# Kernel optimization log

Hardware: AMD Instinct MI355X
Metric: run time of the kernel (lower is better)

## Reference

```python
import jax, jax.numpy as jnp
import numpy as np

EPS = 1e-5

def _bn(x, g, b):
    m = x.mean(axis=0)
    v = x.var(axis=0)  # biased, matches torch BN training normalization
    return g * (x - m) * jax.lax.rsqrt(v + EPS) + b

def _mlp(x, W1, b1, g1, be1, W2, b2, g2, be2):
    h = jax.nn.relu(_bn(x @ W1 + b1, g1, be1))
    return jax.nn.relu(_bn(h @ W2 + b2, g2, be2))

def setup_inputs() -> dict:
    key = jax.random.key(0)
    ks = jax.random.split(key, 12)
    n, e, d, de = 100000, 1600000, 128, 16
    def lin(k, fan_in, fan_out):
        bound = 1.0 / np.sqrt(fan_in)
        k1, k2 = jax.random.split(k)
        W = jax.random.uniform(k1, (fan_in, fan_out), jnp.float32, -bound, bound)
        b = jax.random.uniform(k2, (fan_out,), jnp.float32, -bound, bound)
        return W, b
    msg_W1, msg_b1 = lin(ks[0], 2 * d + de, d)
    msg_W2, msg_b2 = lin(ks[1], d, d)
    upd_W1, upd_b1 = lin(ks[2], 3 * d, d)
    upd_W2, upd_b2 = lin(ks[3], d, d)
    return {
        "h": jax.random.normal(ks[4], (n, d), jnp.float32),
        "edge_index": jax.random.randint(ks[5], (2, e), 0, n, jnp.int64),
        "edge_attr": jax.random.normal(ks[6], (e, de), jnp.float32),
        "msg_W1": msg_W1, "msg_b1": msg_b1,
        "msg_g1": jnp.ones((d,)), "msg_be1": jnp.zeros((d,)),
        "msg_W2": msg_W2, "msg_b2": msg_b2,
        "msg_g2": jnp.ones((d,)), "msg_be2": jnp.zeros((d,)),
        "upd_W1": upd_W1, "upd_b1": upd_b1,
        "upd_g1": jnp.ones((d,)), "upd_be1": jnp.zeros((d,)),
        "upd_W2": upd_W2, "upd_b2": upd_b2,
        "upd_g2": jnp.ones((d,)), "upd_be2": jnp.zeros((d,)),
    }

def reference(h, edge_index, edge_attr,
              msg_W1, msg_b1, msg_g1, msg_be1, msg_W2, msg_b2, msg_g2, msg_be2,
              upd_W1, upd_b1, upd_g1, upd_be1, upd_W2, upd_b2, upd_g2, upd_be2):
    alpha = 0.5
    n = h.shape[0]
    src = edge_index[0]
    dst = edge_index[1]
    h_i = h[src]  # (e, d)
    h_j = h[dst]  # (e, d)
    msg_args = (msg_W1, msg_b1, msg_g1, msg_be1, msg_W2, msg_b2, msg_g2, msg_be2)
    m_st = _mlp(jnp.concatenate([h_i, h_j, edge_attr], axis=-1), *msg_args)
    m_ts = _mlp(jnp.concatenate([h_j, h_i, edge_attr], axis=-1), *msg_args)
    # NOTE: original code scatters both directions by source nodes (faithful)
    a_st = jax.ops.segment_sum(m_st, src, num_segments=n)
    a_ts = jax.ops.segment_sum(m_ts, src, num_segments=n)
    upd_in = jnp.concatenate([h, alpha * a_st, (1.0 - alpha) * a_ts], axis=-1)
    return _mlp(upd_in, upd_W1, upd_b1, upd_g1, upd_be1, upd_W2, upd_b2, upd_g2, upd_be2)
```

## Files before the change

kernel.cpp:

```cpp
#include <hip/hip_runtime.h>

#define EPS_BN 1e-5f

typedef __bf16 bf16x8 __attribute__((ext_vector_type(8)));
typedef _Float16 h4 __attribute__((ext_vector_type(4)));
typedef _Float16 h8 __attribute__((ext_vector_type(8)));
typedef float f32x4 __attribute__((ext_vector_type(4)));
typedef unsigned short us8 __attribute__((ext_vector_type(8)));
typedef unsigned short us4 __attribute__((ext_vector_type(4)));
typedef unsigned int u32x4 __attribute__((ext_vector_type(4)));

__device__ __forceinline__ unsigned short f2bf(float x) {
  unsigned u = __builtin_bit_cast(unsigned, x);
  unsigned r = (u + 0x7fffu + ((u >> 16) & 1u)) >> 16;
  return (unsigned short)r;
}
__device__ __forceinline__ unsigned pack2bf(float a, float b) {
  return (unsigned)f2bf(a) | ((unsigned)f2bf(b) << 16);
}
__device__ __forceinline__ unsigned short f2h(float x) {
  return __builtin_bit_cast(unsigned short, (_Float16)x);
}
__device__ __forceinline__ unsigned pack2h(float a, float b) {
  return (unsigned)f2h(a) | ((unsigned)f2h(b) << 16);
}
__device__ __forceinline__ float ubf(unsigned short u) {
  return __builtin_bit_cast(float, (unsigned)u << 16);
}
__device__ __forceinline__ h4 relu4(h4 x) {
  h4 z = {(_Float16)0.f, (_Float16)0.f, (_Float16)0.f, (_Float16)0.f};
  return __builtin_elementwise_max(x, z);
}

__device__ __forceinline__ int fragidx(int k, int c) {
  int nf = c >> 4, lr = c & 15, ks = k >> 5, lq = (k >> 3) & 3, j = k & 7;
  return ((((nf << 2) + ks) << 6) | (lq << 4) | lr) * 8 + j;
}

__global__ __launch_bounds__(256) void prep_all(
    const float* __restrict__ mW1, const float* __restrict__ mW2,
    const float* __restrict__ uW1, const float* __restrict__ uW2,
    unsigned short* __restrict__ wfrag) {
  int b = blockIdx.x;
  if (b == 7) {
    const float* s7 = mW1 + 256 * 128;
    unsigned short* oc = wfrag + 7L * 16384;
    for (int i = threadIdx.x; i < 2048; i += 256) oc[i] = f2h(s7[i]);
    return;
  }
  const float* src;
  float sc = 1.f;
  switch (b) {
    case 0: src = mW1; break;
    case 1: src = mW1 + 16384; break;
    case 2: src = mW2; break;
    case 3: src = uW1; break;
    case 4: src = uW1 + 16384; sc = 0.5f; break;
    case 5: src = uW1 + 32768; sc = 0.5f; break;
    default: src = uW2; break;
  }
  unsigned short* oc = wfrag + (long)b * 16384;
  bool fp16 = (b == 2);
  for (int i = threadIdx.x; i < 16384; i += 256) {
    float v = src[i] * sc;
    oc[fragidx(i >> 7, i & 127)] = fp16 ? f2h(v) : f2bf(v);
  }
}

__global__ __launch_bounds__(256) void hist_kernel(
    const int* __restrict__ SRC, long E, int* __restrict__ counts) {
  long i = (long)blockIdx.x * 256 + threadIdx.x;
  long str = (long)gridDim.x * 256;
  for (; i < E; i += str) atomicAdd(&counts[SRC[i]], 1);
}

__global__ __launch_bounds__(256) void scan1(
    const int* __restrict__ counts, int n, int* __restrict__ tmp,
    int* __restrict__ bsum) {
  __shared__ int sd[256];
  int b = blockIdx.x, tid = threadIdx.x;
  int base = b * 1024 + tid * 4;
  int c[4], t = 0;
  #pragma unroll
  for (int j = 0; j < 4; ++j) {
    int idx = base + j;
    c[j] = (idx < n) ? counts[idx] : 0;
    t += c[j];
  }
  sd[tid] = t;
  __syncthreads();
  for (int off = 1; off < 256; off <<= 1) {
    int v = (tid >= off) ? sd[tid - off] : 0;
    __syncthreads();
    sd[tid] += v;
    __syncthreads();
  }
  int run = sd[tid] - t;
  #pragma unroll
  for (int j = 0; j < 4; ++j) {
    int idx = base + j;
    if (idx < n) tmp[idx] = run;
    run += c[j];
  }
  if (tid == 255) bsum[b] = sd[255];
}

__global__ __launch_bounds__(256) void scan2(int* __restrict__ bsum, int nb) {
  __shared__ int sd[256];
  int tid = threadIdx.x;
  int v = (tid < nb) ? bsum[tid] : 0;
  sd[tid] = v;
  __syncthreads();
  for (int off = 1; off < 256; off <<= 1) {
    int x = (tid >= off) ? sd[tid - off] : 0;
    __syncthreads();
    sd[tid] += x;
    __syncthreads();
  }
  if (tid < nb) bsum[tid] = sd[tid] - v;
}

__global__ __launch_bounds__(256) void scan3(
    const int* __restrict__ tmp, const int* __restrict__ bsum, int n,
    int* __restrict__ cursor) {
  int i = blockIdx.x * 256 + threadIdx.x;
  if (i < n) cursor[i] = tmp[i] + bsum[i >> 10];
}

__global__ __launch_bounds__(256) void permute_edges(
    const int* __restrict__ SRC, const int* __restrict__ DST,
    const float* __restrict__ EA, long E, int* __restrict__ cursor,
    int* __restrict__ sS, int* __restrict__ sD,
    unsigned short* __restrict__ EAh) {
  long i = (long)blockIdx.x * 256 + threadIdx.x;
  long str = (long)gridDim.x * 256;
  for (; i < E; i += str) {
    int s = SRC[i];
    int pos = atomicAdd(&cursor[s], 1);
    sS[pos] = s;
    sD[pos] = DST[i];
    const float4* ep = (const float4*)(EA + i * 16);
    float4 a = ep[0], b = ep[1], c = ep[2], d = ep[3];
    u32x4 lo, hi;
    lo[0] = pack2h(a.x, a.y); lo[1] = pack2h(a.z, a.w);
    lo[2] = pack2h(b.x, b.y); lo[3] = pack2h(b.z, b.w);
    hi[0] = pack2h(c.x, c.y); hi[1] = pack2h(c.z, c.w);
    hi[2] = pack2h(d.x, d.y); hi[3] = pack2h(d.z, d.w);
    *(u32x4*)(EAh + (long)pos * 16) = lo;
    *(u32x4*)(EAh + (long)pos * 16 + 8) = hi;
  }
}

__global__ __launch_bounds__(256) void node_mfma_pq(
    const float* __restrict__ h, const unsigned short* __restrict__ WfA,
    unsigned short* __restrict__ pqb, int n) {
  __shared__ unsigned short WT[16384];
  int tid = threadIdx.x;
  int lid = tid & 63, w = tid >> 6, lr = lid & 15, lq = lid >> 4;
  long rbase = (long)blockIdx.x * 64 + 16 * w;
  long r = rbase + lr;
  bool rv = (r < n);
  long rl = rv ? r : 0;
  const us8* WF8 = (const us8*)WT;

  bf16x8 af[4];
  const float* Ar = h + rl * 128;
  #pragma unroll
  for (int ks = 0; ks < 4; ++ks) {
    int e0 = 32 * ks + 8 * lq;
    float4 x = *(const float4*)(Ar + e0);
    float4 y = *(const float4*)(Ar + e0 + 4);
    u32x4 t;
    t[0] = pack2bf(x.x, x.y); t[1] = pack2bf(x.z, x.w);
    t[2] = pack2bf(y.x, y.y); t[3] = pack2bf(y.z, y.w);
    if (!rv) { t[0] = 0; t[1] = 0; t[2] = 0; t[3] = 0; }
    af[ks] = __builtin_bit_cast(bf16x8, t);
  }

  f32x4 accP[8], accQ[8];
  #pragma unroll
  for (int nf = 0; nf < 8; ++nf) {
    accP[nf] = f32x4{0.f, 0.f, 0.f, 0.f};
    accQ[nf] = f32x4{0.f, 0.f, 0.f, 0.f};
  }

  for (int i = tid; i < 2048; i += 256) ((us8*)WT)[i] = ((const us8*)WfA)[i];
  __syncthreads();
  #pragma unroll
  for (int nf = 0; nf < 8; ++nf) {
    #pragma unroll
    for (int ks = 0; ks < 4; ++ks) {
      bf16x8 bf = __builtin_bit_cast(bf16x8, WF8[(nf * 4 + ks) * 64 + lid]);
      accP[nf] = __builtin_amdgcn_mfma_f32_16x16x32_bf16(af[ks], bf, accP[nf], 0, 0, 0);
    }
  }
  __syncthreads();
  for (int i = tid; i < 2048; i += 256) ((us8*)WT)[i] = ((const us8*)(WfA + 16384))[i];
  __syncthreads();
  #pragma unroll
  for (int nf = 0; nf < 8; ++nf) {
    #pragma unroll
    for (int ks = 0; ks < 4; ++ks) {
      bf16x8 bf = __builtin_bit_cast(bf16x8, WF8[(nf * 4 + ks) * 64 + lid]);
      accQ[nf] = __builtin_amdgcn_mfma_f32_16x16x32_bf16(af[ks], bf, accQ[nf], 0, 0, 0);
    }
  }

  #pragma unroll
  for (int nf = 0; nf < 8; ++nf) {
    #pragma unroll
    for (int i = 0; i < 4; ++i) {
      long nd = rbase + 4 * lq + i;
      if (nd < n) {
        int ch = 16 * nf + lr;
        pqb[nd * 256 + ch] = f2h(accP[nf][i]);
        pqb[nd * 256 + 128 + ch] = f2h(accQ[nf][i]);
      }
    }
  }
}

template <bool ABF16>
__global__ __launch_bounds__(256) void node_mfma(
    const void* A0, const void* A1, const void* A2,
    const unsigned short* __restrict__ Wf,
    float* __restrict__ C, int n, int dostats,
    float* __restrict__ sum_out, float* __restrict__ ssq_out, int nk) {
  __shared__ unsigned short WT[16384];
  int tid = threadIdx.x;
  int lid = tid & 63, w = tid >> 6, lr = lid & 15, lq = lid >> 4;
  long rbase = (long)blockIdx.x * 64 + 16 * w;

  const void* As[3] = {A0, A1, A2};
  f32x4 acc[8];
  #pragma unroll
  for (int nf = 0; nf < 8; ++nf) acc[nf] = f32x4{0.f, 0.f, 0.f, 0.f};

  long r = rbase + lr;
  bool rv = (r < n);
  long rl = rv ? r : 0;
  const us8* WF8 = (const us8*)WT;

  for (int c = 0; c < nk; ++c) {
    if (c) __syncthreads();
    const us8* src = (const us8*)(Wf + (long)c * 16384);
    for (int i = tid; i < 2048; i += 256) ((us8*)WT)[i] = src[i];
    __syncthreads();

    bf16x8 af[4];
    if (ABF16) {
      const us8* Ar = (const us8*)((const unsigned short*)As[c] + rl * 128);
      #pragma unroll
      for (int ks = 0; ks < 4; ++ks) {
        us8 v = Ar[ks * 4 + lq];
        if (!rv) v = us8{0, 0, 0, 0, 0, 0, 0, 0};
        af[ks] = __builtin_bit_cast(bf16x8, v);
      }
    } else {
      const float* Ar = (const float*)As[c] + rl * 128;
      #pragma unroll
      for (int ks = 0; ks < 4; ++ks) {
        int e0 = 32 * ks + 8 * lq;
        float4 x = *(const float4*)(Ar + e0);
        float4 y = *(const float4*)(Ar + e0 + 4);
        u32x4 t;
        t[0] = pack2bf(x.x, x.y); t[1] = pack2bf(x.z, x.w);
        t[2] = pack2bf(y.x, y.y); t[3] = pack2bf(y.z, y.w);
        if (!rv) { t[0] = 0; t[1] = 0; t[2] = 0; t[3] = 0; }
        af[ks] = __builtin_bit_cast(bf16x8, t);
      }
    }
    #pragma unroll
    for (int nf = 0; nf < 8; ++nf) {
      #pragma unroll
      for (int ks = 0; ks < 4; ++ks) {
        bf16x8 bf = __builtin_bit_cast(bf16x8, WF8[(nf * 4 + ks) * 64 + lid]);
        acc[nf] = __builtin_amdgcn_mfma_f32_16x16x32_bf16(af[ks], bf, acc[nf], 0, 0, 0);
      }
    }
  }

  float lsum[8], lssq[8];
  #pragma unroll
  for (int nf = 0; nf < 8; ++nf) { lsum[nf] = 0.f; lssq[nf] = 0.f; }
  #pragma unroll
  for (int nf = 0; nf < 8; ++nf) {
    #pragma unroll
    for (int i = 0; i < 4; ++i) {
      long nd = rbase + 4 * lq + i;
      if (nd < n) {
        float v = acc[nf][i];
        C[nd * 128 + 16 * nf + lr] = v;
        lsum[nf] += v; lssq[nf] += v * v;
      }
    }
  }
  if (dostats) {
    #pragma unroll
    for (int nf = 0; nf < 8; ++nf) {
      float v0 = lsum[nf]; v0 += __shfl_xor(v0, 16); v0 += __shfl_xor(v0, 32);
      float v1 = lssq[nf]; v1 += __shfl_xor(v1, 16); v1 += __shfl_xor(v1, 32);
      if (lq == 0) {
        atomicAdd(&sum_out[16 * nf + lr], v0);
        atomicAdd(&ssq_out[16 * nf + lr], v1);
      }
    }
  }
}

__global__ __launch_bounds__(256) void msg_stats1b(
    const unsigned short* __restrict__ PQ,
    const unsigned short* __restrict__ EAh, const float* __restrict__ W1e,
    const int* __restrict__ SRC, const int* __restrict__ DST, long E,
    float* __restrict__ stats) {
  __shared__ float Wel[16][128];
  __shared__ float red[32][16];
  int tid = threadIdx.x;
  for (int i = tid; i < 16 * 128; i += 256) ((float*)Wel)[i] = W1e[i];
  for (int i = tid; i < 512; i += 256) ((float*)red)[i] = 0.f;
  __syncthreads();
  int c4 = tid & 31, grp = tid >> 5;
  float4 s_st = {0,0,0,0}, q_st = {0,0,0,0}, s_ts = {0,0,0,0}, q_ts = {0,0,0,0};
  long stride = (long)gridDim.x * 8;
  for (long e = (long)blockIdx.x * 8 + grp; e < E; e += stride) {
    int s = SRC[e], t = DST[e];
    const unsigned short* Rs = PQ + (long)s * 256;
    const unsigned short* Rt = PQ + (long)t * 256;
    h4 Ps = __builtin_bit_cast(h4, *(const us4*)(Rs + 4 * c4));
    h4 Qs = __builtin_bit_cast(h4, *(const us4*)(Rs + 128 + 4 * c4));
    h4 Pt = __builtin_bit_cast(h4, *(const us4*)(Rt + 4 * c4));
    h4 Qt = __builtin_bit_cast(h4, *(const us4*)(Rt + 128 + 4 * c4));
    h8 elo = __builtin_bit_cast(h8, *(const us8*)(EAh + e * 16));
    h8 ehi = __builtin_bit_cast(h8, *(const us8*)(EAh + e * 16 + 8));
    float rx = 0.f, ry = 0.f, rz = 0.f, rw = 0.f;
    #pragma unroll
    for (int k = 0; k < 16; ++k) {
      float f = (k < 8) ? (float)elo[k & 7] : (float)ehi[k & 7];
      const float4 w4 = *(const float4*)&Wel[k][c4 * 4];
      rx = fmaf(f, w4.x, rx); ry = fmaf(f, w4.y, ry);
      rz = fmaf(f, w4.z, rz); rw = fmaf(f, w4.w, rw);
    }
    float zx = (float)Ps[0] + (float)Qt[0] + rx, zy = (float)Ps[1] + (float)Qt[1] + ry;
    float zz = (float)Ps[2] + (float)Qt[2] + rz, zw = (float)Ps[3] + (float)Qt[3] + rw;
    s_st.x += zx; s_st.y += zy; s_st.z += zz; s_st.w += zw;
    q_st.x += zx * zx; q_st.y += zy * zy; q_st.z += zz * zz; q_st.w += zw * zw;
    float ux = (float)Pt[0] + (float)Qs[0] + rx, uy = (float)Pt[1] + (float)Qs[1] + ry;
    float uz = (float)Pt[2] + (float)Qs[2] + rz, uw = (float)Pt[3] + (float)Qs[3] + rw;
    s_ts.x += ux; s_ts.y += uy; s_ts.z += uz; s_ts.w += uw;
    q_ts.x += ux * ux; q_ts.y += uy * uy; q_ts.z += uz * uz; q_ts.w += uw * uw;
  }
  atomicAdd(&red[c4][0], s_st.x);  atomicAdd(&red[c4][1], s_st.y);
  atomicAdd(&red[c4][2], s_st.z);  atomicAdd(&red[c4][3], s_st.w);
  atomicAdd(&red[c4][4], q_st.x);  atomicAdd(&red[c4][5], q_st.y);
  atomicAdd(&red[c4][6], q_st.z);  atomicAdd(&red[c4][7], q_st.w);
  atomicAdd(&red[c4][8], s_ts.x);  atomicAdd(&red[c4][9], s_ts.y);
  atomicAdd(&red[c4][10], s_ts.z); atomicAdd(&red[c4][11], s_ts.w);
  atomicAdd(&red[c4][12], q_ts.x); atomicAdd(&red[c4][13], q_ts.y);
  atomicAdd(&red[c4][14], q_ts.z); atomicAdd(&red[c4][15], q_ts.w);
  __syncthreads();
  #pragma unroll
  for (int rep = 0; rep < 2; ++rep) {
    int j = rep * 256 + tid;
    int cc = j >> 4, k = j & 15, group = k >> 2, comp = k & 3;
    atomicAdd(&stats[group * 128 + cc * 4 + comp], red[cc][k]);
  }
}

template <bool SCATTER>
__global__ __launch_bounds__(256) void msg_mfma10(
    const unsigned short* __restrict__ PQ,
    const unsigned short* __restrict__ EAh,
    const unsigned short* __restrict__ Weh,
    const unsigned short* __restrict__ W2f,
    const int* __restrict__ SRC, const int* __restrict__ DST, long E,
    const float* __restrict__ sc1, const float* __restrict__ sc2,
    float* __restrict__ stats2,
    float* __restrict__ a_st, float* __restrict__ a_ts) {
  __shared__ unsigned short W2F[16384];
  __shared__ unsigned short Atile[2][2][32][136];
  __shared__ int sArr[2][32];

  int tid = threadIdx.x;
  int c4 = tid & 31;
  int slot = tid >> 5;
  int lid = tid & 63, w = tid >> 6, lr = lid & 15, lq = lid >> 4;
  int dir = w >> 1;
  int half = (w & 1) * 16;

  for (int i = tid; i < 2048; i += 256) ((us8*)W2F)[i] = ((const us8*)W2f)[i];
  const us8* W2F8 = (const us8*)W2F;

  h4 wreg[16];
  #pragma unroll
  for (int k = 0; k < 16; ++k)
    wreg[k] = __builtin_bit_cast(h4, *(const us4*)(Weh + k * 128 + c4 * 4));

  int ch0 = c4 * 4;
  h4 scst4 = {(_Float16)sc1[ch0], (_Float16)sc1[ch0 + 1],
              (_Float16)sc1[ch0 + 2], (_Float16)sc1[ch0 + 3]};
  h4 shst4 = {(_Float16)sc1[128 + ch0], (_Float16)sc1[128 + ch0 + 1],
              (_Float16)sc1[128 + ch0 + 2], (_Float16)sc1[128 + ch0 + 3]};
  h4 scts4 = {(_Float16)sc1[256 + ch0], (_Float16)sc1[256 + ch0 + 1],
              (_Float16)sc1[256 + ch0 + 2], (_Float16)sc1[256 + ch0 + 3]};
  h4 shts4 = {(_Float16)sc1[384 + ch0], (_Float16)sc1[384 + ch0 + 1],
              (_Float16)sc1[384 + ch0 + 2], (_Float16)sc1[384 + ch0 + 3]};

  float s2[8], h2p[8];
  float ssum[8], sssq[8];
  if constexpr (SCATTER) {
    const float* scd = sc2 + dir * 256;
    #pragma unroll
    for (int nf = 0; nf < 8; ++nf) {
      int ch = 16 * nf + lr;
      s2[nf] = scd[ch]; h2p[nf] = scd[128 + ch];
    }
  } else {
    #pragma unroll
    for (int nf = 0; nf < 8; ++nf) { ssum[nf] = 0.f; sssq[nf] = 0.f; }
  }
  float* accOut = dir ? a_ts : a_st;

  long tb0 = (long)blockIdx.x * 32;
  long tstep = (long)gridDim.x * 32;

  auto phaseA = [&](long tb, int p) {
    int nE = (int)(E - tb < 32 ? E - tb : 32);
    #pragma unroll
    for (int rep = 0; rep < 4; ++rep) {
      int er = rep * 8 + slot;
      if (er < nE) {
        long e = tb + er;
        int s = SRC[e], t = DST[e];
        if (SCATTER && c4 == 0) sArr[p][er] = s;
        const us4* Rs = (const us4*)(PQ + (long)s * 256);
        const us4* Rt = (const us4*)(PQ + (long)t * 256);
        h4 Ps = __builtin_bit_cast(h4, Rs[c4]);
        h4 Qs = __builtin_bit_cast(h4, Rs[32 + c4]);
        h4 Pt = __builtin_bit_cast(h4, Rt[c4]);
        h4 Qt = __builtin_bit_cast(h4, Rt[32 + c4]);
        h8 elo = __builtin_bit_cast(h8, *(const us8*)(EAh + e * 16));
        h8 ehi = __builtin_bit_cast(h8, *(const us8*)(EAh + e * 16 + 8));
        h4 r = {(_Float16)0.f, (_Float16)0.f, (_Float16)0.f, (_Float16)0.f};
        #pragma unroll
        for (int k = 0; k < 16; ++k) {
          _Float16 f = (k < 8) ? elo[k & 7] : ehi[k & 7];
          h4 fv = {f, f, f, f};
          r += fv * wreg[k];
        }
        h4 zst = relu4((Ps + Qt + r) * scst4 + shst4);
        h4 zts = relu4((Pt + Qs + r) * scts4 + shts4);
        *(unsigned long long*)&Atile[p][0][er][ch0] =
            __builtin_bit_cast(unsigned long long, zst);
        *(unsigned long long*)&Atile[p][1][er][ch0] =
            __builtin_bit_cast(unsigned long long, zts);
      } else {
        *(unsigned long long*)&Atile[p][0][er][ch0] = 0ull;
        *(unsigned long long*)&Atile[p][1][er][ch0] = 0ull;
      }
    }
  };

  if (tb0 < E) phaseA(tb0, 0);
  __syncthreads();

  int p = 0;
  for (long tb = tb0; tb < E; tb += tstep) {
    int nE = (int)(E - tb < 32 ? E - tb : 32);
    long tnext = tb + tstep;

    int arow = half + lr;
    const char* ap = (const char*)&Atile[p][dir][arow][0];
    int acolb = lq * 16;
    h8 af[4];
    #pragma unroll
    for (int ks = 0; ks < 4; ++ks) {
      af[ks] = *(const h8*)(ap + ks * 64 + acolb);
    }
    int srow[4];
    bool uniform = false;
    int usrc = -1;
    if constexpr (SCATTER) {
      #pragma unroll
      for (int i = 0; i < 4; ++i) {
        int row = half + 4 * lq + i;
        srow[i] = (row < nE) ? sArr[p][row] : -1;
      }
      if (half + 15 < nE) {
        usrc = sArr[p][half];
        uniform = (usrc == sArr[p][half + 15]);
      }
    }
    f32x4 acc[8];
    __builtin_amdgcn_s_setprio(1);
    #pragma unroll
    for (int nf = 0; nf < 8; ++nf) {
      acc[nf] = f32x4{0.f, 0.f, 0.f, 0.f};
      #pragma unroll
      for (int ks = 0; ks < 4; ++ks) {
        h8 bf = __builtin_bit_cast(h8, W2F8[(nf * 4 + ks) * 64 + lid]);
        acc[nf] = __builtin_amdgcn_mfma_f32_16x16x32_f16(af[ks], bf, acc[nf], 0, 0, 0);
      }
    }
    __builtin_amdgcn_s_setprio(0);

    if (tnext < E) phaseA(tnext, p ^ 1);

    #pragma unroll
    for (int nf = 0; nf < 8; ++nf) {
      if constexpr (SCATTER) {
        int ch = 16 * nf + lr;
        if (uniform) {
          float m = 0.f;
          #pragma unroll
          for (int i = 0; i < 4; ++i)
            m += fmaxf(fmaf(acc[nf][i], s2[nf], h2p[nf]), 0.f);
          m += __shfl_xor(m, 16);
          m += __shfl_xor(m, 32);
          if (lq == 0 && m != 0.f)
            atomicAdd(&accOut[(long)usrc * 128 + ch], m);
        } else {
          int cur = srow[0];
          float m = fmaxf(fmaf(acc[nf][0], s2[nf], h2p[nf]), 0.f);
          #pragma unroll
          for (int i = 1; i < 4; ++i) {
            float v = fmaxf(fmaf(acc[nf][i], s2[nf], h2p[nf]), 0.f);
            if (srow[i] == cur) {
              m += v;
            } else {
              if (cur >= 0 && m != 0.f) atomicAdd(&accOut[(long)cur * 128 + ch], m);
              cur = srow[i]; m = v;
            }
          }
          if (cur >= 0 && m != 0.f) atomicAdd(&accOut[(long)cur * 128 + ch], m);
        }
      } else {
        #pragma unroll
        for (int i = 0; i < 4; ++i) {
          ssum[nf] += acc[nf][i]; sssq[nf] += acc[nf][i] * acc[nf][i];
        }
      }
    }
    __syncthreads();
    p ^= 1;
  }

  if constexpr (!SCATTER) {
    #pragma unroll
    for (int nf = 0; nf < 8; ++nf) {
      float v0 = ssum[nf]; v0 += __shfl_xor(v0, 16); v0 += __shfl_xor(v0, 32);
      float v1 = sssq[nf]; v1 += __shfl_xor(v1, 16); v1 += __shfl_xor(v1, 32);
      if (lq == 0) {
        int ch = 16 * nf + lr;
        atomicAdd(&stats2[dir * 256 + ch], v0);
        atomicAdd(&stats2[dir * 256 + 128 + ch], v1);
      }
    }
  }
}

__global__ void bn_finalize(const float* __restrict__ sum, const float* __restrict__ ssq,
                            float invN, const float* __restrict__ g,
                            const float* __restrict__ be,
                            float* __restrict__ sc, float* __restrict__ sh) {
  int j = threadIdx.x;
  float m = sum[j] * invN;
  float v = ssq[j] * invN - m * m;
  float s = g[j] * rsqrtf(v + EPS_BN);
  sc[j] = s;
  sh[j] = be[j] - m * s;
}

__global__ __launch_bounds__(256) void prescale_relu(
    const float* __restrict__ X, const float* __restrict__ scsh,
    unsigned* __restrict__ out, long nrows) {
  long gid = (long)blockIdx.x * 256 + threadIdx.x;
  int c2 = (int)(gid & 63);
  float s0 = scsh[2 * c2], s1 = scsh[2 * c2 + 1];
  float h0 = scsh[128 + 2 * c2], h1 = scsh[128 + 2 * c2 + 1];
  const float2* X2 = (const float2*)X;
  long rstride = ((long)gridDim.x * 256) >> 6;
  for (long row = gid >> 6; row < nrows; row += rstride) {
    float2 x = X2[row * 64 + c2];
    out[row * 64 + c2] = pack2bf(fmaxf(fmaf(x.x, s0, h0), 0.f),
                                 fmaxf(fmaf(x.y, s1, h1), 0.f));
  }
}

__global__ __launch_bounds__(256) void bn_relu_out(
    const float* __restrict__ U2, const float* __restrict__ scsh,
    float* __restrict__ out, long total) {
  long i = (long)blockIdx.x * blockDim.x + threadIdx.x;
  long stride = (long)gridDim.x * blockDim.x;
  for (; i < total; i += stride) {
    int j = (int)(i & 127);
    out[i] = fmaxf(fmaf(U2[i], scsh[j], scsh[128 + j]), 0.f);
  }
}

extern "C" void kernel_launch(void* const* d_in, const int* in_sizes, int n_in,
                              void* d_out, int out_size, void* d_ws, size_t ws_size,
                              hipStream_t stream) {
  const float* h    = (const float*)d_in[0];
  const int*   ei   = (const int*)d_in[1];
  const float* ea   = (const float*)d_in[2];
  const float* mW1  = (const float*)d_in[3];
  const float* mg1  = (const float*)d_in[5];
  const float* mbe1 = (const float*)d_in[6];
  const float* mW2  = (const float*)d_in[7];
  const float* mg2  = (const float*)d_in[9];
  const float* mbe2 = (const float*)d_in[10];
  const float* uW1  = (const float*)d_in[11];
  const float* ug1  = (const float*)d_in[13];
  const float* ube1 = (const float*)d_in[14];
  const float* uW2  = (const float*)d_in[15];
  const float* ug2  = (const float*)d_in[17];
  const float* ube2 = (const float*)d_in[18];

  int n = in_sizes[0] / 128;
  long E = (long)(in_sizes[1] / 2);
  const int* SRC = ei;
  const int* DST = ei + E;
  const float* W1e = mW1 + 256 * 128;

  size_t nf = (size_t)n * 128;
  unsigned short* pqb = (unsigned short*)d_ws;
  float* a_st = (float*)(pqb + (size_t)n * 256);
  float* a_ts = a_st + nf;
  float* st   = a_ts + nf;
  unsigned short* wfrag = (unsigned short*)(st + 3072);
  unsigned short* wfA  = wfrag;
  unsigned short* wfW2 = wfrag + 2 * 16384;
  unsigned short* wfU1 = wfrag + 3 * 16384;
  unsigned short* wfU2 = wfrag + 6 * 16384;
  unsigned short* wfWe = wfrag + 7 * 16384;
  int* sS = (int*)(wfWe + 2048);
  int* sD = sS + E;
  unsigned short* EAh = (unsigned short*)(sD + E);
  int* counts = (int*)(EAh + (size_t)E * 16);
  int* tmp = counts + n;
  int* bsum = tmp + n;

  float invE = 1.0f / (float)E;
  float invN = 1.0f / (float)n;
  int nblk = (n + 63) / 64;
  int nb1 = (n + 1023) / 1024;

  prep_all<<<8, 256, 0, stream>>>(mW1, mW2, uW1, uW2, wfrag);
  hipMemsetAsync(st, 0, 3072 * sizeof(float), stream);
  hipMemsetAsync(a_st, 0, 2 * nf * sizeof(float), stream);
  hipMemsetAsync(counts, 0, (size_t)n * sizeof(int), stream);

  hist_kernel<<<1024, 256, 0, stream>>>(SRC, E, counts);
  scan1<<<nb1, 256, 0, stream>>>(counts, n, tmp, bsum);
  scan2<<<1, 256, 0, stream>>>(bsum, nb1);
  scan3<<<(n + 255) / 256, 256, 0, stream>>>(tmp, bsum, n, counts);
  permute_edges<<<1024, 256, 0, stream>>>(SRC, DST, ea, E, counts, sS, sD, EAh);

  node_mfma_pq<<<nblk, 256, 0, stream>>>(h, wfA, pqb, n);

  msg_stats1b<<<2048, 256, 0, stream>>>(pqb, EAh, W1e, sS, sD, E, st);
  bn_finalize<<<1, 128, 0, stream>>>(st + 0,   st + 128, invE, mg1, mbe1, st + 1536, st + 1664);
  bn_finalize<<<1, 128, 0, stream>>>(st + 256, st + 384, invE, mg1, mbe1, st + 1792, st + 1920);

  msg_mfma10<false><<<1536, 256, 0, stream>>>(
      pqb, EAh, wfWe, wfW2, sS, sD, E, st + 1536, nullptr, st + 512, nullptr, nullptr);
  bn_finalize<<<1, 128, 0, stream>>>(st + 512, st + 640, invE, mg2, mbe2, st + 2048, st + 2176);
  bn_finalize<<<1, 128, 0, stream>>>(st + 768, st + 896, invE, mg2, mbe2, st + 2304, st + 2432);

  msg_mfma10<true><<<1536, 256, 0, stream>>>(
      pqb, EAh, wfWe, wfW2, sS, sD, E, st + 1536, st + 2048, nullptr, a_st, a_ts);

  float* u1 = (float*)pqb;
  node_mfma<false><<<nblk, 256, 0, stream>>>(h, a_st, a_ts, wfU1,
                                             u1, n, 1, st + 1024, st + 1152, 3);
  bn_finalize<<<1, 128, 0, stream>>>(st + 1024, st + 1152, invN, ug1, ube1, st + 2560, st + 2688);

  unsigned short* u1p = (unsigned short*)a_st;
  float* u2 = a_ts;
  prescale_relu<<<2048, 256, 0, stream>>>(u1, st + 2560, (unsigned*)u1p, n);
  node_mfma<true><<<nblk, 256, 0, stream>>>(u1p, nullptr, nullptr, wfU2,
                                            u2, n, 1, st + 1280, st + 1408, 1);
  bn_finalize<<<1, 128, 0, stream>>>(st + 1280, st + 1408, invN, ug2, ube2, st + 2816, st + 2944);

  bn_relu_out<<<2048, 256, 0, stream>>>(u2, st + 2816, (float*)d_out, (long)n * 128);
}
```

Measured before the change: 2.435 ms.

## Materialize second-layer message activations to avoid recomputing edge MLP for scatter

```diff
diff --git a/kernel.cpp b/kernel.cpp
--- a/kernel.cpp
+++ b/kernel.cpp
@@ -364,6 +364,184 @@
     int cc = j >> 4, k = j & 15, group = k >> 2, comp = k & 3;
     atomicAdd(&stats[group * 128 + cc * 4 + comp], red[cc][k]);
   }
+}
+
+__global__ __launch_bounds__(256) void msg_mfma11(
+    const unsigned short* __restrict__ PQ,
+    const unsigned short* __restrict__ EAh,
+    const unsigned short* __restrict__ Weh,
+    const unsigned short* __restrict__ W2f,
+    const int* __restrict__ SRC, const int* __restrict__ DST, long E,
+    const float* __restrict__ sc1, float* __restrict__ stats2,
+    unsigned short* __restrict__ ybuf) {
+  __shared__ unsigned short W2F[16384];
+  __shared__ unsigned short Atile[2][2][32][136];
+
+  int tid = threadIdx.x;
+  int c4 = tid & 31;
+  int slot = tid >> 5;
+  int lid = tid & 63, w = tid >> 6, lr = lid & 15, lq = lid >> 4;
+  int dir = w >> 1;
+  int half = (w & 1) * 16;
+
+  for (int i = tid; i < 2048; i += 256) ((us8*)W2F)[i] = ((const us8*)W2f)[i];
+  const us8* W2F8 = (const us8*)W2F;
+
+  h4 wreg[16];
+  #pragma unroll
+  for (int k = 0; k < 16; ++k)
+    wreg[k] = __builtin_bit_cast(h4, *(const us4*)(Weh + k * 128 + c4 * 4));
+
+  int ch0 = c4 * 4;
+  h4 scst4 = {(_Float16)sc1[ch0], (_Float16)sc1[ch0 + 1],
+              (_Float16)sc1[ch0 + 2], (_Float16)sc1[ch0 + 3]};
+  h4 shst4 = {(_Float16)sc1[128 + ch0], (_Float16)sc1[128 + ch0 + 1],
+              (_Float16)sc1[128 + ch0 + 2], (_Float16)sc1[128 + ch0 + 3]};
+  h4 scts4 = {(_Float16)sc1[256 + ch0], (_Float16)sc1[256 + ch0 + 1],
+              (_Float16)sc1[256 + ch0 + 2], (_Float16)sc1[256 + ch0 + 3]};
+  h4 shts4 = {(_Float16)sc1[384 + ch0], (_Float16)sc1[384 + ch0 + 1],
+              (_Float16)sc1[384 + ch0 + 2], (_Float16)sc1[384 + ch0 + 3]};
+
+  float ssum[8], sssq[8];
+  #pragma unroll
+  for (int nf = 0; nf < 8; ++nf) { ssum[nf] = 0.f; sssq[nf] = 0.f; }
+
+  long tb0 = (long)blockIdx.x * 32;
+  long tstep = (long)gridDim.x * 32;
+
+  auto phaseA = [&](long tb, int p) {
+    int nE = (int)(E - tb < 32 ? E - tb : 32);
+    #pragma unroll
+    for (int rep = 0; rep < 4; ++rep) {
+      int er = rep * 8 + slot;
+      if (er < nE) {
+        long e = tb + er;
+        int s = SRC[e], t = DST[e];
+        const us4* Rs = (const us4*)(PQ + (long)s * 256);
+        const us4* Rt = (const us4*)(PQ + (long)t * 256);
+        h4 Ps = __builtin_bit_cast(h4, Rs[c4]);
+        h4 Qs = __builtin_bit_cast(h4, Rs[32 + c4]);
+        h4 Pt = __builtin_bit_cast(h4, Rt[c4]);
+        h4 Qt = __builtin_bit_cast(h4, Rt[32 + c4]);
+        h8 elo = __builtin_bit_cast(h8, *(const us8*)(EAh + e * 16));
+        h8 ehi = __builtin_bit_cast(h8, *(const us8*)(EAh + e * 16 + 8));
+        h4 r = {(_Float16)0.f, (_Float16)0.f, (_Float16)0.f, (_Float16)0.f};
+        #pragma unroll
+        for (int k = 0; k < 16; ++k) {
+          _Float16 f = (k < 8) ? elo[k & 7] : ehi[k & 7];
+          h4 fv = {f, f, f, f};
+          r += fv * wreg[k];
+        }
+        h4 zst = relu4((Ps + Qt + r) * scst4 + shst4);
+        h4 zts = relu4((Pt + Qs + r) * scts4 + shts4);
+        *(unsigned long long*)&Atile[p][0][er][ch0] =
+            __builtin_bit_cast(unsigned long long, zst);
+        *(unsigned long long*)&Atile[p][1][er][ch0] =
+            __builtin_bit_cast(unsigned long long, zts);
+      } else {
+        *(unsigned long long*)&Atile[p][0][er][ch0] = 0ull;
+        *(unsigned long long*)&Atile[p][1][er][ch0] = 0ull;
+      }
+    }
+  };
+
+  if (tb0 < E) phaseA(tb0, 0);
+  __syncthreads();
+
+  int p = 0;
+  for (long tb = tb0; tb < E; tb += tstep) {
+    int nE = (int)(E - tb < 32 ? E - tb : 32);
+    long tnext = tb + tstep;
+
+    int arow = half + lr;
+    const char* ap = (const char*)&Atile[p][dir][arow][0];
+    int acolb = lq * 16;
+    h8 af[4];
+    #pragma unroll
+    for (int ks = 0; ks < 4; ++ks) {
+      af[ks] = *(const h8*)(ap + ks * 64 + acolb);
+    }
+    f32x4 acc[8];
+    __builtin_amdgcn_s_setprio(1);
+    #pragma unroll
+    for (int nf = 0; nf < 8; ++nf) {
+      acc[nf] = f32x4{0.f, 0.f, 0.f, 0.f};
+      #pragma unroll
+      for (int ks = 0; ks < 4; ++ks) {
+        h8 bf = __builtin_bit_cast(h8, W2F8[(nf * 4 + ks) * 64 + lid]);
+        acc[nf] = __builtin_amdgcn_mfma_f32_16x16x32_f16(af[ks], bf, acc[nf], 0, 0, 0);
+      }
+    }
+    __builtin_amdgcn_s_setprio(0);
+
+    if (tnext < E) phaseA(tnext, p ^ 1);
+
+    #pragma unroll
+    for (int nf = 0; nf < 8; ++nf) {
+      int ch = 16 * nf + lr;
+      #pragma unroll
+      for (int i = 0; i < 4; ++i) {
+        float v = acc[nf][i];
+        ssum[nf] += v; sssq[nf] += v * v;
+        int row = half + 4 * lq + i;
+        if (row < nE) ybuf[(tb + row) * 256 + dir * 128 + ch] = f2h(v);
+      }
+    }
+    __syncthreads();
+    p ^= 1;
+  }
+
+  #pragma unroll
+  for (int nf = 0; nf < 8; ++nf) {
+    float v0 = ssum[nf]; v0 += __shfl_xor(v0, 16); v0 += __shfl_xor(v0, 32);
+    float v1 = sssq[nf]; v1 += __shfl_xor(v1, 16); v1 += __shfl_xor(v1, 32);
+    if (lq == 0) {
+      int ch = 16 * nf + lr;
+      atomicAdd(&stats2[dir * 256 + ch], v0);
+      atomicAdd(&stats2[dir * 256 + 128 + ch], v1);
+    }
+  }
+}
+
+__global__ __launch_bounds__(256) void scatter_stream(
+    const unsigned short* __restrict__ Y, const int* __restrict__ sS, long E,
+    const float* __restrict__ sc2,
+    float* __restrict__ a_st, float* __restrict__ a_ts) {
+  __shared__ unsigned short Yl[8][256];
+  __shared__ int Sl[8];
+  int tid = threadIdx.x;
+  int dir = tid >> 7, ch = tid & 127;
+  float s2 = sc2[dir * 256 + ch];
+  float h2 = sc2[dir * 256 + 128 + ch];
+  float* accOut = dir ? a_ts : a_st;
+  long eper = (E + gridDim.x - 1) / gridDim.x;
+  long e0 = (long)blockIdx.x * eper;
+  long e1 = e0 + eper; if (e1 > E) e1 = E;
+  int run_src = -1;
+  float run_acc = 0.f;
+  for (long cb = e0; cb < e1; cb += 8) {
+    int cnt = (int)((e1 - cb < 8) ? (e1 - cb) : 8);
+    int le = tid >> 5, lo = (tid & 31) * 8;
+    if (le < cnt)
+      *(us8*)&Yl[le][lo] = *(const us8*)(Y + (cb + le) * 256 + lo);
+    if (tid < cnt) Sl[tid] = sS[cb + tid];
+    __syncthreads();
+    for (int i = 0; i < cnt; ++i) {
+      float y = (float)__builtin_bit_cast(_Float16, Yl[i][dir * 128 + ch]);
+      float v = fmaxf(fmaf(y, s2, h2), 0.f);
+      int s = Sl[i];
+      if (s == run_src) {
+        run_acc += v;
+      } else {
+        if (run_src >= 0 && run_acc != 0.f)
+          atomicAdd(&accOut[(long)run_src * 128 + ch], run_acc);
+        run_src = s; run_acc = v;
+      }
+    }
+    __syncthreads();
+  }
+  if (run_src >= 0 && run_acc != 0.f)
+    atomicAdd(&accOut[(long)run_src * 128 + ch], run_acc);
 }
 
 template <bool SCATTER>
@@ -639,6 +817,9 @@
   int* counts = (int*)(EAh + (size_t)E * 16);
   int* tmp = counts + n;
   int* bsum = tmp + n;
+  unsigned short* ybuf = (unsigned short*)(bsum + 256);
+  size_t needY = (size_t)((char*)(ybuf + (size_t)E * 256) - (char*)d_ws);
+  bool matY = (ws_size >= needY);
 
   float invE = 1.0f / (float)E;
   float invN = 1.0f / (float)n;
@@ -662,13 +843,20 @@
   bn_finalize<<<1, 128, 0, stream>>>(st + 0,   st + 128, invE, mg1, mbe1, st + 1536, st + 1664);
   bn_finalize<<<1, 128, 0, stream>>>(st + 256, st + 384, invE, mg1, mbe1, st + 1792, st + 1920);
 
-  msg_mfma10<false><<<1536, 256, 0, stream>>>(
-      pqb, EAh, wfWe, wfW2, sS, sD, E, st + 1536, nullptr, st + 512, nullptr, nullptr);
-  bn_finalize<<<1, 128, 0, stream>>>(st + 512, st + 640, invE, mg2, mbe2, st + 2048, st + 2176);
-  bn_finalize<<<1, 128, 0, stream>>>(st + 768, st + 896, invE, mg2, mbe2, st + 2304, st + 2432);
-
-  msg_mfma10<true><<<1536, 256, 0, stream>>>(
-      pqb, EAh, wfWe, wfW2, sS, sD, E, st + 1536, st + 2048, nullptr, a_st, a_ts);
+  if (matY) {
+    msg_mfma11<<<1536, 256, 0, stream>>>(
+        pqb, EAh, wfWe, wfW2, sS, sD, E, st + 1536, st + 512, ybuf);
+    bn_finalize<<<1, 128, 0, stream>>>(st + 512, st + 640, invE, mg2, mbe2, st + 2048, st + 2176);
+    bn_finalize<<<1, 128, 0, stream>>>(st + 768, st + 896, invE, mg2, mbe2, st + 2304, st + 2432);
+    scatter_stream<<<2048, 256, 0, stream>>>(ybuf, sS, E, st + 2048, a_st, a_ts);
+  } else {
+    msg_mfma10<false><<<1536, 256, 0, stream>>>(
+        pqb, EAh, wfWe, wfW2, sS, sD, E, st + 1536, nullptr, st + 512, nullptr, nullptr);
+    bn_finalize<<<1, 128, 0, stream>>>(st + 512, st + 640, invE, mg2, mbe2, st + 2048, st + 2176);
+    bn_finalize<<<1, 128, 0, stream>>>(st + 768, st + 896, invE, mg2, mbe2, st + 2304, st + 2432);
+    msg_mfma10<true><<<1536, 256, 0, stream>>>(
+        pqb, EAh, wfWe, wfW2, sS, sD, E, st + 1536, st + 2048, nullptr, a_st, a_ts);
+  }
 
   float* u1 = (float*)pqb;
   node_mfma<false><<<nblk, 256, 0, stream>>>(h, a_st, a_ts, wfU1,
```

After: 2.426 ms. No clear change (-0.4%).

## Precompute edge-attribute projection into workspace buffer and use streamlined message kernels

Applied to the files above, without the earlier changes.

```diff
diff --git a/kernel.cpp b/kernel.cpp
--- a/kernel.cpp
+++ b/kernel.cpp
@@ -24,11 +24,13 @@
 __device__ __forceinline__ unsigned pack2h(float a, float b) {
   return (unsigned)f2h(a) | ((unsigned)f2h(b) << 16);
 }
-__device__ __forceinline__ float ubf(unsigned short u) {
-  return __builtin_bit_cast(float, (unsigned)u << 16);
-}
 __device__ __forceinline__ h4 relu4(h4 x) {
   h4 z = {(_Float16)0.f, (_Float16)0.f, (_Float16)0.f, (_Float16)0.f};
+  return __builtin_elementwise_max(x, z);
+}
+__device__ __forceinline__ h8 relu8(h8 x) {
+  h8 z = {(_Float16)0.f, (_Float16)0.f, (_Float16)0.f, (_Float16)0.f,
+          (_Float16)0.f, (_Float16)0.f, (_Float16)0.f, (_Float16)0.f};
   return __builtin_elementwise_max(x, z);
 }
 
@@ -363,6 +365,182 @@
     int j = rep * 256 + tid;
     int cc = j >> 4, k = j & 15, group = k >> 2, comp = k & 3;
     atomicAdd(&stats[group * 128 + cc * 4 + comp], red[cc][k]);
+  }
+}
+
+__global__ __launch_bounds__(256) void rmat_raw(
+    const unsigned short* __restrict__ EAh, const unsigned short* __restrict__ Weh,
+    unsigned short* __restrict__ R, long cbase, long csz) {
+  long gid = (long)blockIdx.x * 256 + threadIdx.x;
+  int c2 = (int)(gid & 63);
+  int ch = 2 * c2;
+  float wa[16], wb[16];
+  #pragma unroll
+  for (int k = 0; k < 16; ++k) {
+    wa[k] = (float)__builtin_bit_cast(_Float16, Weh[k * 128 + ch]);
+    wb[k] = (float)__builtin_bit_cast(_Float16, Weh[k * 128 + ch + 1]);
+  }
+  long estride = ((long)gridDim.x * 256) >> 6;
+  for (long e = gid >> 6; e < csz; e += estride) {
+    h8 elo = __builtin_bit_cast(h8, *(const us8*)(EAh + (cbase + e) * 16));
+    h8 ehi = __builtin_bit_cast(h8, *(const us8*)(EAh + (cbase + e) * 16 + 8));
+    float ra = 0.f, rb = 0.f;
+    #pragma unroll
+    for (int k = 0; k < 16; ++k) {
+      float f = (k < 8) ? (float)elo[k & 7] : (float)ehi[k & 7];
+      ra = fmaf(f, wa[k], ra); rb = fmaf(f, wb[k], rb);
+    }
+    ((unsigned*)R)[e * 64 + c2] = pack2h(ra, rb);
+  }
+}
+
+template <bool SCATTER>
+__global__ __launch_bounds__(256) void msg_bf(
+    const unsigned short* __restrict__ PQ,
+    const unsigned short* __restrict__ Rr,
+    const unsigned short* __restrict__ W2f,
+    const int* __restrict__ SRC, const int* __restrict__ DST,
+    long cbase, long csz,
+    const float* __restrict__ sc1, const float* __restrict__ sc2,
+    float* __restrict__ stats2,
+    float* __restrict__ a_st, float* __restrict__ a_ts) {
+  __shared__ unsigned short W2F[16384];
+  int tid = threadIdx.x;
+  int lid = tid & 63, w = tid >> 6, lr = lid & 15, lq = lid >> 4;
+  int dir = w >> 1;
+  int half = (w & 1) * 16;
+
+  for (int i = tid; i < 2048; i += 256) ((us8*)W2F)[i] = ((const us8*)W2f)[i];
+  const us8* W2F8 = (const us8*)W2F;
+
+  const float* scd = sc1 + dir * 256;
+  h8 scr[4], shr[4];
+  #pragma unroll
+  for (int ks = 0; ks < 4; ++ks) {
+    int c0 = 32 * ks + 8 * lq;
+    h8 a, b;
+    #pragma unroll
+    for (int j = 0; j < 8; ++j) {
+      a[j] = (_Float16)scd[c0 + j];
+      b[j] = (_Float16)scd[128 + c0 + j];
+    }
+    scr[ks] = a; shr[ks] = b;
+  }
+
+  float s2[8], h2p[8], ssum[8], sssq[8];
+  if constexpr (SCATTER) {
+    const float* s = sc2 + dir * 256;
+    #pragma unroll
+    for (int nf = 0; nf < 8; ++nf) {
+      int ch = 16 * nf + lr;
+      s2[nf] = s[ch]; h2p[nf] = s[128 + ch];
+    }
+  } else {
+    #pragma unroll
+    for (int nf = 0; nf < 8; ++nf) { ssum[nf] = 0.f; sssq[nf] = 0.f; }
+  }
+  float* accOut = dir ? a_ts : a_st;
+
+  int offS = dir ? 128 : 0;
+  int offD = dir ? 0 : 128;
+  __syncthreads();
+
+  for (long wb0 = (long)blockIdx.x * 32 + half; wb0 < csz;
+       wb0 += (long)gridDim.x * 32) {
+    long le = wb0 + lr;
+    bool ev = (le < csz);
+    long lel = ev ? le : (csz - 1);
+    long ge = cbase + lel;
+    int s = SRC[ge], t = DST[ge];
+    const us8* SrcH = (const us8*)(PQ + (long)s * 256 + offS);
+    const us8* DstH = (const us8*)(PQ + (long)t * 256 + offD);
+    const us8* Rrow = (const us8*)(Rr + lel * 128);
+
+    h8 af[4];
+    #pragma unroll
+    for (int ks = 0; ks < 4; ++ks) {
+      int ci = ks * 4 + lq;
+      h8 ps = __builtin_bit_cast(h8, SrcH[ci]);
+      h8 qd = __builtin_bit_cast(h8, DstH[ci]);
+      h8 rr = __builtin_bit_cast(h8, Rrow[ci]);
+      h8 z = relu8((ps + qd + rr) * scr[ks] + shr[ks]);
+      if (!ev) {
+        h8 zr = {(_Float16)0.f, (_Float16)0.f, (_Float16)0.f, (_Float16)0.f,
+                 (_Float16)0.f, (_Float16)0.f, (_Float16)0.f, (_Float16)0.f};
+        z = zr;
+      }
+      af[ks] = z;
+    }
+
+    int srow[4];
+    bool uniform = false;
+    int usrc = -1;
+    if constexpr (SCATTER) {
+      #pragma unroll
+      for (int i = 0; i < 4; ++i) {
+        long rowe = wb0 + 4 * lq + i;
+        srow[i] = (rowe < csz) ? SRC[cbase + rowe] : -1;
+      }
+      if (wb0 + 15 < csz) {
+        usrc = SRC[cbase + wb0];
+        uniform = (usrc == SRC[cbase + wb0 + 15]);
+      }
+    }
+
+    #pragma unroll
+    for (int nf = 0; nf < 8; ++nf) {
+      f32x4 acc = {0.f, 0.f, 0.f, 0.f};
+      #pragma unroll
+      for (int ks = 0; ks < 4; ++ks) {
+        h8 bf = __builtin_bit_cast(h8, W2F8[(nf * 4 + ks) * 64 + lid]);
+        acc = __builtin_amdgcn_mfma_f32_16x16x32_f16(af[ks], bf, acc, 0, 0, 0);
+      }
+      if constexpr (SCATTER) {
+        int ch = 16 * nf + lr;
+        if (uniform) {
+          float m = 0.f;
+          #pragma unroll
+          for (int i = 0; i < 4; ++i)
+            m += fmaxf(fmaf(acc[i], s2[nf], h2p[nf]), 0.f);
+          m += __shfl_xor(m, 16);
+          m += __shfl_xor(m, 32);
+          if (lq == 0 && m != 0.f)
+            atomicAdd(&accOut[(long)usrc * 128 + ch], m);
+        } else {
+          int cur = srow[0];
+          float m = fmaxf(fmaf(acc[0], s2[nf], h2p[nf]), 0.f);
+          #pragma unroll
+          for (int i = 1; i < 4; ++i) {
+            float v = fmaxf(fmaf(acc[i], s2[nf], h2p[nf]), 0.f);
+            if (srow[i] == cur) {
+              m += v;
+            } else {
+              if (cur >= 0 && m != 0.f) atomicAdd(&accOut[(long)cur * 128 + ch], m);
+              cur = srow[i]; m = v;
+            }
+          }
+          if (cur >= 0 && m != 0.f) atomicAdd(&accOut[(long)cur * 128 + ch], m);
+        }
+      } else {
+        #pragma unroll
+        for (int i = 0; i < 4; ++i) {
+          ssum[nf] += acc[i]; sssq[nf] += acc[i] * acc[i];
+        }
+      }
+    }
+  }
+
+  if constexpr (!SCATTER) {
+    #pragma unroll
+    for (int nf = 0; nf < 8; ++nf) {
+      float v0 = ssum[nf]; v0 += __shfl_xor(v0, 16); v0 += __shfl_xor(v0, 32);
+      float v1 = sssq[nf]; v1 += __shfl_xor(v1, 16); v1 += __shfl_xor(v1, 32);
+      if (lq == 0) {
+        int ch = 16 * nf + lr;
+        atomicAdd(&stats2[dir * 256 + ch], v0);
+        atomicAdd(&stats2[dir * 256 + 128 + ch], v1);
+      }
+    }
   }
 }
 
@@ -639,6 +817,13 @@
   int* counts = (int*)(EAh + (size_t)E * 16);
   int* tmp = counts + n;
   int* bsum = tmp + n;
+  unsigned short* Rbuf = (unsigned short*)(bsum + 256);
+  size_t used = (size_t)((char*)Rbuf - (char*)d_ws);
+  long rcap = (ws_size > used) ? (long)((ws_size - used) / 256) : 0;
+  long CHUNK = rcap & ~63L;
+  if (CHUNK > E) CHUNK = E;
+  bool bf = (CHUNK >= 400000);
+  bool rfull = (CHUNK >= E);
 
   float invE = 1.0f / (float)E;
   float invN = 1.0f / (float)n;
@@ -662,13 +847,46 @@
   bn_finalize<<<1, 128, 0, stream>>>(st + 0,   st + 128, invE, mg1, mbe1, st + 1536, st + 1664);
   bn_finalize<<<1, 128, 0, stream>>>(st + 256, st + 384, invE, mg1, mbe1, st + 1792, st + 1920);
 
-  msg_mfma10<false><<<1536, 256, 0, stream>>>(
-      pqb, EAh, wfWe, wfW2, sS, sD, E, st + 1536, nullptr, st + 512, nullptr, nullptr);
-  bn_finalize<<<1, 128, 0, stream>>>(st + 512, st + 640, invE, mg2, mbe2, st + 2048, st + 2176);
-  bn_finalize<<<1, 128, 0, stream>>>(st + 768, st + 896, invE, mg2, mbe2, st + 2304, st + 2432);
-
-  msg_mfma10<true><<<1536, 256, 0, stream>>>(
-      pqb, EAh, wfWe, wfW2, sS, sD, E, st + 1536, st + 2048, nullptr, a_st, a_ts);
+  if (bf) {
+    if (rfull) {
+      rmat_raw<<<2048, 256, 0, stream>>>(EAh, wfWe, Rbuf, 0, E);
+      int g = (int)(((E + 31) / 32 < 2048) ? (E + 31) / 32 : 2048);
+      msg_bf<false><<<g, 256, 0, stream>>>(pqb, Rbuf, wfW2, sS, sD, 0, E,
+                                           st + 1536, nullptr, st + 512,
+                                           nullptr, nullptr);
+      bn_finalize<<<1, 128, 0, stream>>>(st + 512, st + 640, invE, mg2, mbe2, st + 2048, st + 2176);
+      bn_finalize<<<1, 128, 0, stream>>>(st + 768, st + 896, invE, mg2, mbe2, st + 2304, st + 2432);
+      msg_bf<true><<<g, 256, 0, stream>>>(pqb, Rbuf, wfW2, sS, sD, 0, E,
+                                          st + 1536, st + 2048, nullptr,
+                                          a_st, a_ts);
+    } else {
+      for (long cb = 0; cb < E; cb += CHUNK) {
+        long csz = (E - cb < CHUNK) ? (E - cb) : CHUNK;
+        rmat_raw<<<2048, 256, 0, stream>>>(EAh, wfWe, Rbuf, cb, csz);
+        int g = (int)(((csz + 31) / 32 < 2048) ? (csz + 31) / 32 : 2048);
+        msg_bf<false><<<g, 256, 0, stream>>>(pqb, Rbuf, wfW2, sS, sD, cb, csz,
+                                             st + 1536, nullptr, st + 512,
+                                             nullptr, nullptr);
+      }
+      bn_finalize<<<1, 128, 0, stream>>>(st + 512, st + 640, invE, mg2, mbe2, st + 2048, st + 2176);
+      bn_finalize<<<1, 128, 0, stream>>>(st + 768, st + 896, invE, mg2, mbe2, st + 2304, st + 2432);
+      for (long cb = 0; cb < E; cb += CHUNK) {
+        long csz = (E - cb < CHUNK) ? (E - cb) : CHUNK;
+        rmat_raw<<<2048, 256, 0, stream>>>(EAh, wfWe, Rbuf, cb, csz);
+        int g = (int)(((csz + 31) / 32 < 2048) ? (csz + 31) / 32 : 2048);
+        msg_bf<true><<<g, 256, 0, stream>>>(pqb, Rbuf, wfW2, sS, sD, cb, csz,
+                                            st + 1536, st + 2048, nullptr,
+                                            a_st, a_ts);
+      }
+    }
+  } else {
+    msg_mfma10<false><<<1536, 256, 0, stream>>>(
+        pqb, EAh, wfWe, wfW2, sS, sD, E, st + 1536, nullptr, st + 512, nullptr, nullptr);
+    bn_finalize<<<1, 128, 0, stream>>>(st + 512, st + 640, invE, mg2, mbe2, st + 2048, st + 2176);
+    bn_finalize<<<1, 128, 0, stream>>>(st + 768, st + 896, invE, mg2, mbe2, st + 2304, st + 2432);
+    msg_mfma10<true><<<1536, 256, 0, stream>>>(
+        pqb, EAh, wfWe, wfW2, sS, sD, E, st + 1536, st + 2048, nullptr, a_st, a_ts);
+  }
 
   float* u1 = (float*)pqb;
   node_mfma<false><<<nblk, 256, 0, stream>>>(h, a_st, a_ts, wfU1,
```

After: 2.967 ms. +21.8%, slower.
